# Kernel tuning notes

Measured on AMD Instinct MI355X. Metric: run time of the kernel, lower is better.

Reference implementation:

```python
import jax, jax.numpy as jnp
import numpy as np

EPS = 1e-4

@jax.custom_vjp
def binarize(x):
    # BinaryConnectDeterministic: sign with sign(0)=+1
    return jnp.where(x >= 0, 1.0, -1.0).astype(x.dtype)

def _bin_fwd(x):
    return binarize(x), x

def _bin_bwd(x, g):
    # straight-through estimator, clipped to |x| <= 1
    return (g * (jnp.abs(x) <= 1).astype(g.dtype),)

binarize.defvjp(_bin_fwd, _bin_bwd)

def ap2(x):
    # approximate power-of-2: sign(x) * 2^round(log2|x|); grad is 0 a.e. (round/sign)
    a = jnp.maximum(jnp.abs(x), 1e-38)
    return jnp.sign(x) * jnp.exp2(jnp.round(jnp.log2(a)))

def shift_bn(x, gamma, beta, axes):
    # shift-based batch norm (BNN paper): var approximated via centered*AP2(centered),
    # inverse std and gamma replaced by their AP2 approximations. Training-mode batch stats.
    mean = jnp.mean(x, axis=axes, keepdims=True)
    c = x - mean
    var = jnp.mean(c * ap2(c), axis=axes, keepdims=True)
    xhat = c * ap2(1.0 / jnp.sqrt(var + EPS))
    shape = [1] * x.ndim
    shape[1] = x.shape[1]
    return ap2(gamma.reshape(shape)) * xhat + beta.reshape(shape)

def conv_bin(x, w, b):
    y = jax.lax.conv_general_dilated(x, binarize(w), (1, 1), [(1, 1), (1, 1)],
                                     dimension_numbers=('NCHW', 'OIHW', 'NCHW'))
    return y + b[None, :, None, None]

def maxpool3s2(x):
    return jax.lax.reduce_window(x, -jnp.inf, jax.lax.max,
                                 (1, 1, 3, 3), (1, 1, 2, 2), 'VALID')


def setup_inputs() -> dict:
    key = jax.random.key(0)
    ks = jax.random.split(key, 8)
    B, NU = 2048, 2048
    inp = {
        'x': jax.random.normal(ks[0], (B, 784), jnp.float32),
        'conv1_w': jax.random.normal(ks[1], (32, 1, 3, 3), jnp.float32) * 0.1,
        'conv1_b': jnp.zeros((32,), jnp.float32),
        'g1': jnp.ones((32,), jnp.float32), 'b1': jnp.zeros((32,), jnp.float32),
        'conv2_w': jax.random.normal(ks[2], (64, 32, 3, 3), jnp.float32) * 0.1,
        'conv2_b': jnp.zeros((64,), jnp.float32),
        'g2': jnp.ones((64,), jnp.float32), 'b2': jnp.zeros((64,), jnp.float32),
        'lin3_w': jax.random.normal(ks[3], (NU, 10816), jnp.float32) * 0.02,
        'lin3_b': jnp.zeros((NU,), jnp.float32),
        'g3': jnp.ones((NU,), jnp.float32), 'b3': jnp.zeros((NU,), jnp.float32),
        'lin4_w': jax.random.normal(ks[4], (10, NU), jnp.float32) * 0.02,
        'lin4_b': jnp.zeros((10,), jnp.float32),
    }
    return inp


def reference(x, conv1_w, conv1_b, g1, b1, conv2_w, conv2_b, g2, b2,
              lin3_w, lin3_b, g3, b3, lin4_w, lin4_b):
    h = x.reshape(-1, 1, 28, 28)
    h = jax.nn.relu(conv_bin(h, conv1_w, conv1_b))
    h = shift_bn(h, g1, b1, axes=(0, 2, 3))
    h = binarize(h)
    h = jax.nn.relu(conv_bin(h, conv2_w, conv2_b))
    h = maxpool3s2(h)                       # [B,64,13,13]
    h = shift_bn(h, g2, b2, axes=(0, 2, 3))
    h = binarize(h)
    h = h.reshape(h.shape[0], -1)           # [B,10816]
    h = jax.nn.relu(h @ binarize(lin3_w).T + lin3_b)
    h = shift_bn(h, g3, b3, axes=(0,))
    h = binarize(h)
    return h @ binarize(lin4_w).T + lin4_b  # [B,10] (no norm4/logsoftmax in forward)
```

## Files before the change

### kernel.cpp

```cpp
#include <hip/hip_runtime.h>

#define BB 2048
#define IMG 784
#define HWD 28
#define C1 32
#define C2 64
#define PP 169
#define PD 13
#define F3 10816
#define N3 2048
#define K4W 32
#define NOUT 10
#define CONV 27
#define PADW 30
#define OCCHUNK 8
#define IMGC 29
#define SCRP 740

typedef unsigned long long u64;
typedef int v4i __attribute__((ext_vector_type(4)));
typedef int v16i __attribute__((ext_vector_type(16)));

#define GLOAD16(gp, lp) __builtin_amdgcn_global_load_lds( \
    (__attribute__((address_space(1))) void*)(gp),        \
    (__attribute__((address_space(3))) void*)(lp), 16, 0, 0)

__device__ __forceinline__ float ap2mag(float c) {
    unsigned int a = __float_as_uint(c) & 0x7fffffffu;
    unsigned int e = (a >> 23) + ((a & 0x7fffffu) > 0x3504f3u);
    return __uint_as_float(e << 23);
}
__device__ __forceinline__ float ap2sgn(float g) {
    unsigned int u = __float_as_uint(g);
    unsigned int a = u & 0x7fffffffu;
    if (a == 0) return 0.f;
    unsigned int e = (a >> 23) + ((a & 0x7fffffu) > 0x3504f3u);
    return __uint_as_float((u & 0x80000000u) | (e << 23));
}

__global__ __launch_bounds__(256) void stage0(const float* __restrict__ x,
                                              const float* __restrict__ w1, const float* __restrict__ cb1,
                                              float* __restrict__ part1, float* __restrict__ w1b,
                                              const float* __restrict__ w2, char* __restrict__ w2i8,
                                              const float* __restrict__ w3, char* __restrict__ wp3i,
                                              const float* __restrict__ w4, u64* __restrict__ wp4) {
    __shared__ float xs[30 * PADW];
    __shared__ float red[4 * C1];
    int n = blockIdx.x, tid = threadIdx.x;
    int lane = tid & 63, wv = tid >> 6;
    {
        int idx = n * 256 + tid;
        int nthr = gridDim.x * 256;
        int total = (N3 * F3) / 4;
        for (int t = idx; t < total; t += nthr) {
            float4 wv4 = *(const float4*)(w3 + (size_t)t * 4);
            unsigned int w = (wv4.x >= 0.f ? 0x01u : 0xffu)
                           | (wv4.y >= 0.f ? 0x01u : 0xffu) << 8
                           | (wv4.z >= 0.f ? 0x01u : 0xffu) << 16
                           | (wv4.w >= 0.f ? 0x01u : 0xffu) << 24;
            *(unsigned int*)(wp3i + (size_t)t * 4) = w;
        }
    }
    if (n == 0) {
        for (int i = tid; i < C1 * 9; i += 256) w1b[i] = (w1[i] >= 0.f) ? 1.f : -1.f;
    } else if (n == 1) {
        for (int i = tid; i < 2 * 9 * 64 * 16; i += 256) {
            int hf = i / 9216;
            int r = i - hf * 9216;
            int t = r >> 10;
            int l = (r >> 4) & 63;
            int j = i & 15;
            int oc = hf * 32 + (l & 31);
            int ic = ((l >> 5) << 4) + j;
            w2i8[i] = (w2[oc * 288 + ic * 9 + t] >= 0.f) ? (char)1 : (char)(-1);
        }
    } else if (n == 2) {
        for (int w = wv; w < NOUT * K4W; w += 4) {
            int o = w / K4W, j = w % K4W;
            float wvl = w4[o * N3 + j * 64 + lane];
            u64 mask = __ballot(wvl >= 0.f);
            if (lane == 0) wp4[w] = mask;
        }
    }
    for (int i = tid; i < 30 * PADW; i += 256) {
        int r = i / PADW - 1, c = i % PADW - 1;
        float v = 0.f;
        if (r >= 0 && r < HWD && c >= 0 && c < HWD) v = x[n * IMG + r * HWD + c];
        xs[i] = v;
    }
    __syncthreads();
    bool act = tid < 196;
    int r = tid / 7, c0 = (tid % 7) * 4;
    float win[18];
#pragma unroll
    for (int k = 0; k < 18; k++) win[k] = 0.f;
    if (act) {
#pragma unroll
        for (int ry = 0; ry < 3; ry++)
#pragma unroll
            for (int cx = 0; cx < 6; cx++)
                win[ry * 6 + cx] = xs[(r + ry) * PADW + c0 + cx];
    }
#pragma unroll
    for (int ch = 0; ch < C1; ch++) {
        float a = 0.f;
        if (act) {
            float k0 = (w1[ch * 9 + 0] >= 0.f) ? 1.f : -1.f, k1 = (w1[ch * 9 + 1] >= 0.f) ? 1.f : -1.f;
            float k2 = (w1[ch * 9 + 2] >= 0.f) ? 1.f : -1.f, k3 = (w1[ch * 9 + 3] >= 0.f) ? 1.f : -1.f;
            float k4 = (w1[ch * 9 + 4] >= 0.f) ? 1.f : -1.f, k5 = (w1[ch * 9 + 5] >= 0.f) ? 1.f : -1.f;
            float k6 = (w1[ch * 9 + 6] >= 0.f) ? 1.f : -1.f, k7 = (w1[ch * 9 + 7] >= 0.f) ? 1.f : -1.f;
            float k8 = (w1[ch * 9 + 8] >= 0.f) ? 1.f : -1.f;
            float b = cb1[ch];
#pragma unroll
            for (int px = 0; px < 4; px++) {
                float s = win[px] * k0 + win[px + 1] * k1 + win[px + 2] * k2
                        + win[6 + px] * k3 + win[7 + px] * k4 + win[8 + px] * k5
                        + win[12 + px] * k6 + win[13 + px] * k7 + win[14 + px] * k8;
                a += fmaxf(s + b, 0.f);
            }
        }
        for (int off = 32; off; off >>= 1) a += __shfl_down(a, off);
        if (lane == 0) red[wv * C1 + ch] = a;
    }
    __syncthreads();
    if (tid < C1) part1[n * C1 + tid] = red[tid] + red[C1 + tid] + red[2 * C1 + tid] + red[3 * C1 + tid];
}

__global__ __launch_bounds__(256) void conv1_var(const float* __restrict__ x,
                            const float* __restrict__ w1b,
                            const float* __restrict__ cb1, const float* __restrict__ mean1,
                            float* __restrict__ part) {
    __shared__ float xs[30 * PADW];
    __shared__ float red[4 * C1];
    int n = blockIdx.x, tid = threadIdx.x;
    for (int i = tid; i < 30 * PADW; i += 256) {
        int r = i / PADW - 1, c = i % PADW - 1;
        float v = 0.f;
        if (r >= 0 && r < HWD && c >= 0 && c < HWD) v = x[n * IMG + r * HWD + c];
        xs[i] = v;
    }
    __syncthreads();
    bool act = tid < 196;
    int r = tid / 7, c0 = (tid % 7) * 4;
    float win[18];
#pragma unroll
    for (int k = 0; k < 18; k++) win[k] = 0.f;
    if (act) {
#pragma unroll
        for (int ry = 0; ry < 3; ry++)
#pragma unroll
            for (int cx = 0; cx < 6; cx++)
                win[ry * 6 + cx] = xs[(r + ry) * PADW + c0 + cx];
    }
    int lane = tid & 63, wv = tid >> 6;
#pragma unroll
    for (int ch = 0; ch < C1; ch++) {
        float a = 0.f;
        if (act) {
            float k0 = w1b[ch * 9 + 0], k1 = w1b[ch * 9 + 1], k2 = w1b[ch * 9 + 2];
            float k3 = w1b[ch * 9 + 3], k4 = w1b[ch * 9 + 4], k5 = w1b[ch * 9 + 5];
            float k6 = w1b[ch * 9 + 6], k7 = w1b[ch * 9 + 7], k8 = w1b[ch * 9 + 8];
            float b = cb1[ch], m = mean1[ch];
#pragma unroll
            for (int px = 0; px < 4; px++) {
                float s = win[px] * k0 + win[px + 1] * k1 + win[px + 2] * k2
                        + win[6 + px] * k3 + win[7 + px] * k4 + win[8 + px] * k5
                        + win[12 + px] * k6 + win[13 + px] * k7 + win[14 + px] * k8;
                float v = fmaxf(s + b, 0.f);
                float c = v - m;
                a += fabsf(c) * ap2mag(c);
            }
        }
        for (int off = 32; off; off >>= 1) a += __shfl_down(a, off);
        if (lane == 0) red[wv * C1 + ch] = a;
    }
    __syncthreads();
    if (tid < C1) part[n * C1 + tid] = red[tid] + red[C1 + tid] + red[2 * C1 + tid] + red[3 * C1 + tid];
}

__global__ __launch_bounds__(256) void conv1_pack(const float* __restrict__ x,
                           const float* __restrict__ w1b,
                           const float* __restrict__ cb1, const float* __restrict__ mean1,
                           const float* __restrict__ scale1, const float* __restrict__ beta1,
                           unsigned int* __restrict__ s1p) {
    __shared__ float xs[30 * PADW];
    int n = blockIdx.x, tid = threadIdx.x;
    for (int i = tid; i < 30 * PADW; i += 256) {
        int r = i / PADW - 1, c = i % PADW - 1;
        float v = 0.f;
        if (r >= 0 && r < HWD && c >= 0 && c < HWD) v = x[n * IMG + r * HWD + c];
        xs[i] = v;
    }
    __syncthreads();
    if (tid >= 196) return;
    int r = tid / 7, c0 = (tid % 7) * 4;
    float win[18];
#pragma unroll
    for (int ry = 0; ry < 3; ry++)
#pragma unroll
        for (int cx = 0; cx < 6; cx++)
            win[ry * 6 + cx] = xs[(r + ry) * PADW + c0 + cx];
    unsigned int bits0 = 0, bits1 = 0, bits2 = 0, bits3 = 0;
#pragma unroll
    for (int ch = 0; ch < C1; ch++) {
        float k0 = w1b[ch * 9 + 0], k1 = w1b[ch * 9 + 1], k2 = w1b[ch * 9 + 2];
        float k3 = w1b[ch * 9 + 3], k4 = w1b[ch * 9 + 4], k5 = w1b[ch * 9 + 5];
        float k6 = w1b[ch * 9 + 6], k7 = w1b[ch * 9 + 7], k8 = w1b[ch * 9 + 8];
        float b = cb1[ch], m = mean1[ch], sc = scale1[ch], bt = beta1[ch];
#pragma unroll
        for (int px = 0; px < 4; px++) {
            float s = win[px] * k0 + win[px + 1] * k1 + win[px + 2] * k2
                    + win[6 + px] * k3 + win[7 + px] * k4 + win[8 + px] * k5
                    + win[12 + px] * k6 + win[13 + px] * k7 + win[14 + px] * k8;
            float v = fmaxf(s + b, 0.f);
            float val = sc * (v - m) + bt;
            unsigned int bit = (val >= 0.f ? 1u : 0u) << ch;
            if (px == 0) bits0 |= bit;
            else if (px == 1) bits1 |= bit;
            else if (px == 2) bits2 |= bit;
            else bits3 |= bit;
        }
    }
    uint4 w4v = make_uint4(bits0, bits1, bits2, bits3);
    *reinterpret_cast<uint4*>(&s1p[n * IMG + r * HWD + c0]) = w4v;
}

__global__ __launch_bounds__(256) void conv2pool(const unsigned int* __restrict__ s1p,
                                                 const char* __restrict__ w2i8,
                                                 const float* __restrict__ cb2,
                                                 short* __restrict__ p2i,
                                                 float* __restrict__ part2) {
    __shared__ char img[IMGC * IMGC * 32];
    __shared__ short scr[32 * SCRP];
    __shared__ float psum[OCCHUNK * PP];
    __shared__ float pm[C2];
    int n = blockIdx.x, tid = threadIdx.x;
    int lane = tid & 63, wv = tid >> 6;
    for (int i = tid; i < IMGC * IMGC; i += 256) {
        int r = i / IMGC, c = i - r * IMGC;
        unsigned int w = 0u;
        if (r >= 1 && c >= 1) w = s1p[n * IMG + (r - 1) * HWD + (c - 1)];
        unsigned int d[8];
        if (r == 0 || c == 0) {
#pragma unroll
            for (int e = 0; e < 8; e++) d[e] = 0u;
        } else {
#pragma unroll
            for (int e = 0; e < 8; e++) {
                unsigned int nib = (w >> (4 * e)) & 0xFu;
                unsigned int t = (nib & 1u) | ((nib & 2u) << 7) | ((nib & 4u) << 14) | ((nib & 8u) << 21);
                d[e] = 0xFFFFFFFFu - t * 0xFEu;
            }
        }
        *(uint4*)&img[i * 32] = make_uint4(d[0], d[1], d[2], d[3]);
        *(uint4*)&img[i * 32 + 16] = make_uint4(d[4], d[5], d[6], d[7]);
    }
    __syncthreads();
    int hh = lane >> 5;
    int l31 = lane & 31;
    for (int hf = 0; hf < 2; hf++) {
        v4i bf[9];
#pragma unroll
        for (int t = 0; t < 9; t++)
            bf[t] = *(const v4i*)(w2i8 + (hf * 9 + t) * 1024 + lane * 16);
#pragma unroll
        for (int j = 0; j < 3; j++) {
            int mtA = wv + 8 * j, mtB = mtA + 4;
            int pA = mtA * 32 + l31; if (pA > 728) pA = 728;
            int pB = mtB * 32 + l31; if (pB > 728) pB = 728;
            int yA = pA / 27, xA = pA - yA * 27;
            int yB = pB / 27, xB = pB - yB * 27;
            int aA = (yA * IMGC + xA) * 32 + hh * 16;
            int aB = (yB * IMGC + xB) * 32 + hh * 16;
            v16i accA = {0,0,0,0,0,0,0,0,0,0,0,0,0,0,0,0};
            v16i accB = {0,0,0,0,0,0,0,0,0,0,0,0,0,0,0,0};
#pragma unroll
            for (int ky = 0; ky < 3; ky++)
#pragma unroll
                for (int kx = 0; kx < 3; kx++) {
                    v4i fA = *(const v4i*)&img[aA + (ky * IMGC + kx) * 32];
                    v4i fB = *(const v4i*)&img[aB + (ky * IMGC + kx) * 32];
                    accA = __builtin_amdgcn_mfma_i32_32x32x32_i8(fA, bf[ky * 3 + kx], accA, 0, 0, 0);
                    accB = __builtin_amdgcn_mfma_i32_32x32x32_i8(fB, bf[ky * 3 + kx], accB, 0, 0, 0);
                }
            short* sr = &scr[l31 * SCRP];
#pragma unroll
            for (int g = 0; g < 4; g++) {
                short4 sA;
                sA.x = (short)accA[4 * g + 0]; sA.y = (short)accA[4 * g + 1];
                sA.z = (short)accA[4 * g + 2]; sA.w = (short)accA[4 * g + 3];
                *(short4*)&sr[mtA * 32 + g * 8 + 4 * hh] = sA;
            }
            if (mtB < 23) {
#pragma unroll
                for (int g = 0; g < 4; g++) {
                    short4 sB;
                    sB.x = (short)accB[4 * g + 0]; sB.y = (short)accB[4 * g + 1];
                    sB.z = (short)accB[4 * g + 2]; sB.w = (short)accB[4 * g + 3];
                    *(short4*)&sr[mtB * 32 + g * 8 + 4 * hh] = sB;
                }
            }
        }
        __syncthreads();
        for (int base = 0; base < 32; base += OCCHUNK) {
            for (int q = tid; q < OCCHUNK * PP; q += 256) {
                int ol = q / PP, pix = q - ol * PP;
                int py = pix / PD, px = pix - py * PD;
                const short* rr = &scr[(base + ol) * SCRP + (2 * py) * CONV + 2 * px];
                int m0 = max(max((int)rr[0], (int)rr[1]), (int)rr[2]);
                int m1 = max(max((int)rr[CONV], (int)rr[CONV + 1]), (int)rr[CONV + 2]);
                int m2 = max(max((int)rr[2 * CONV], (int)rr[2 * CONV + 1]), (int)rr[2 * CONV + 2]);
                int val = max(max(m0, m1), m2);
                int oc = hf * 32 + base + ol;
                p2i[n * F3 + oc * PP + pix] = (short)val;
                psum[q] = fmaxf((float)val + cb2[oc], 0.f);
            }
            __syncthreads();
            for (int ol = wv; ol < OCCHUNK; ol += 4) {
                float a = 0.f;
                for (int pp = lane; pp < PP; pp += 64) a += psum[ol * PP + pp];
                for (int off = 32; off; off >>= 1) a += __shfl_down(a, off);
                if (lane == 0) pm[hf * 32 + base + ol] = a;
            }
            __syncthreads();
        }
    }
    if (tid < C2) part2[n * C2 + tid] = pm[tid];
}

__global__ __launch_bounds__(256) void p2_var(const short* __restrict__ p2i,
                         const float* __restrict__ cb2,
                         const float* __restrict__ mean2, float* __restrict__ part) {
    int n = blockIdx.x, tid = threadIdx.x, lane = tid & 63, wv = tid >> 6;
    const short* rowb = p2i + (size_t)n * F3;
    __shared__ float red[C2];
#pragma unroll
    for (int i = 0; i < 16; i++) {
        int ch = wv * 16 + i;
        const short* row = rowb + ch * PP;
        float b = cb2[ch];
        float m = mean2[ch];
        float a = 0.f;
        for (int p = lane; p < PP; p += 64) {
            float v = fmaxf((float)row[p] + b, 0.f);
            float c = v - m;
            a += fabsf(c) * ap2mag(c);
        }
        for (int off = 32; off; off >>= 1) a += __shfl_down(a, off);
        if (lane == 0) red[ch] = a;
    }
    __syncthreads();
    if (tid < C2) part[n * C2 + tid] = red[tid];
}

__global__ __launch_bounds__(256) void reduce_stats(const float* __restrict__ part, int nch, int nblk,
                             const float* __restrict__ g, float* __restrict__ outv,
                             int mode, double count) {
    int ch = blockIdx.x, tid = threadIdx.x;
    double a = 0.0;
    for (int i = tid; i < nblk; i += 256) a += (double)part[(size_t)i * nch + ch];
    __shared__ double red[4];
    for (int off = 32; off; off >>= 1) a += __shfl_down(a, off);
    int lane = tid & 63, wv = tid >> 6;
    if (lane == 0) red[wv] = a;
    __syncthreads();
    if (tid == 0) {
        double s = red[0] + red[1] + red[2] + red[3];
        if (mode == 0) {
            outv[ch] = (float)(s / count);
        } else {
            float var = (float)(s / count);
            float inv = 1.0f / sqrtf(var + 1e-4f);
            outv[ch] = ap2sgn(g[ch]) * ap2mag(inv);
        }
    }
}

__global__ __launch_bounds__(256) void p2_packi8(const short* __restrict__ p2i, const float* __restrict__ cb2,
                        const float* __restrict__ mean2, const float* __restrict__ scale2,
                        const float* __restrict__ beta2, char* __restrict__ hp3i) {
    int idx = blockIdx.x * 256 + threadIdx.x;
    int nthr = gridDim.x * 256;
    int total = (BB * F3) / 4;
    for (int t = idx; t < total; t += nthr) {
        int base = t * 4;
        int f0 = base % F3;
        unsigned int w = 0;
#pragma unroll
        for (int e = 0; e < 4; e++) {
            int f = f0 + e;
            int oc = f / PP;
            float v = fmaxf((float)p2i[base + e] + cb2[oc], 0.f);
            float val = scale2[oc] * (v - mean2[oc]) + beta2[oc];
            w |= (val >= 0.f ? 0x01u : 0xffu) << (8 * e);
        }
        *(unsigned int*)(hp3i + base) = w;
    }
}

__global__ __launch_bounds__(256) void lin3_mfma(const char* __restrict__ hp3i,
                                                 const char* __restrict__ wp3i,
                                                 const float* __restrict__ b3l,
                                                 float* __restrict__ h3,
                                                 float* __restrict__ h3T,
                                                 float* __restrict__ part3) {
    __shared__ v4i aL[2][1024];
    __shared__ v4i bL[2][512];
    __shared__ float csr[4][32];
    int tid = threadIdx.x;
    int lane = tid & 63, wv = tid >> 6;
    int wr = wv >> 1, wc = wv & 1;
    int m0 = blockIdx.y * 128, n0 = blockIdx.x * 64;
    int loff = (lane & 15) * F3 + (lane >> 4) * 16;
    const char* gA0 = hp3i + (size_t)(m0 + wv * 16) * F3 + loff;
    const char* gA1 = gA0 + (size_t)64 * F3;
    const char* gB0 = wp3i + (size_t)(n0 + wv * 16) * F3 + loff;
    char* ldsA = (char*)&aL[0][0];
    char* ldsB = (char*)&bL[0][0];
    int sA = wv * 1024, sB = wv * 1024;
    v4i acc[4][2];
#pragma unroll
    for (int i = 0; i < 4; i++)
#pragma unroll
        for (int j = 0; j < 2; j++) acc[i][j] = (v4i){0, 0, 0, 0};
    GLOAD16(gA0,      ldsA + sA);
    GLOAD16(gA1,      ldsA + sA + 4096);
    GLOAD16(gA0 + 64, ldsA + sA + 8192);
    GLOAD16(gA1 + 64, ldsA + sA + 12288);
    GLOAD16(gB0,      ldsB + sB);
    GLOAD16(gB0 + 64, ldsB + sB + 4096);
    __syncthreads();
    for (int c = 0; c <= 84; ++c) {
        int cur = c & 1;
        if (c < 84) {
            int nb = cur ^ 1;
            const char* pA0 = gA0 + (size_t)(c + 1) * 128;
            const char* pA1 = gA1 + (size_t)(c + 1) * 128;
            const char* pB0 = gB0 + (size_t)(c + 1) * 128;
            char* dA = ldsA + nb * 16384 + sA;
            char* dB = ldsB + nb * 8192 + sB;
            GLOAD16(pA0, dA);
            GLOAD16(pA1, dA + 4096);
            GLOAD16(pB0, dB);
            if (c + 1 < 84) {
                GLOAD16(pA0 + 64, dA + 8192);
                GLOAD16(pA1 + 64, dA + 12288);
                GLOAD16(pB0 + 64, dB + 4096);
            }
        }
        const v4i* aC = &aL[cur][0];
        const v4i* bC = &bL[cur][0];
        int nks = (c == 84) ? 1 : 2;
        for (int ks = 0; ks < nks; ++ks) {
            v4i af[4], bf[2];
#pragma unroll
            for (int i = 0; i < 4; i++) af[i] = aC[ks * 512 + (wr * 4 + i) * 64 + lane];
#pragma unroll
            for (int j = 0; j < 2; j++) bf[j] = bC[ks * 256 + (wc * 2 + j) * 64 + lane];
#pragma unroll
            for (int i = 0; i < 4; i++)
#pragma unroll
                for (int j = 0; j < 2; j++)
                    acc[i][j] = __builtin_amdgcn_mfma_i32_16x16x64_i8(af[i], bf[j], acc[i][j], 0, 0, 0);
        }
        __syncthreads();
    }
    int q = lane >> 4, m16 = lane & 15;
    float cs[2] = {0.f, 0.f};
#pragma unroll
    for (int j = 0; j < 2; j++) {
        int col = n0 + wc * 32 + j * 16 + m16;
        float bias = b3l[col];
#pragma unroll
        for (int i = 0; i < 4; i++) {
            int rowb = m0 + wr * 64 + i * 16 + q * 4;
            float4 t4;
#pragma unroll
            for (int rg = 0; rg < 4; rg++) {
                float v = fmaxf((float)acc[i][j][rg] + bias, 0.f);
                h3[(size_t)(rowb + rg) * N3 + col] = v;
                ((float*)&t4)[rg] = v;
                cs[j] += v;
            }
            *(float4*)&h3T[(size_t)col * BB + rowb] = t4;
        }
    }
#pragma unroll
    for (int j = 0; j < 2; j++) {
        cs[j] += __shfl_xor(cs[j], 16);
        cs[j] += __shfl_xor(cs[j], 32);
        if (lane < 16) csr[wv][j * 16 + m16] = cs[j];
    }
    __syncthreads();
    if (tid < 64) {
        int wcc = tid >> 5, cc = tid & 31;
        part3[(size_t)blockIdx.y * N3 + n0 + tid] = csr[wcc][cc] + csr[2 + wcc][cc];
    }
}

__global__ __launch_bounds__(256) void h3_finish(const float* __restrict__ h3T,
                                                 const float* __restrict__ part3,
                                                 const float* __restrict__ g3,
                                                 float* __restrict__ mean3, float* __restrict__ scale3) {
    int nn = blockIdx.x, tid = threadIdx.x;
    __shared__ float msh;
    __shared__ double redd[4];
    if (tid < 64) {
        float a = (tid < 16) ? part3[(size_t)tid * N3 + nn] : 0.f;
        for (int off = 8; off; off >>= 1) a += __shfl_down(a, off);
        if (tid == 0) { float m = a / (float)BB; mean3[nn] = m; msh = m; }
    }
    __syncthreads();
    float m = msh;
    float acc = 0.f;
#pragma unroll
    for (int q = 0; q < 8; q++) {
        float v = h3T[(size_t)nn * BB + q * 256 + tid];
        float c = v - m;
        acc += fabsf(c) * ap2mag(c);
    }
    double a = (double)acc;
    for (int off = 32; off; off >>= 1) a += __shfl_down(a, off);
    int lane = tid & 63, wv = tid >> 6;
    if (lane == 0) redd[wv] = a;
    __syncthreads();
    if (tid == 0) {
        float var = (float)((redd[0] + redd[1] + redd[2] + redd[3]) / (double)BB);
        float inv = 1.0f / sqrtf(var + 1e-4f);
        scale3[nn] = ap2sgn(g3[nn]) * ap2mag(inv);
    }
}

__global__ __launch_bounds__(256) void h4_out(const float* __restrict__ h3,
                                              const float* __restrict__ mean3, const float* __restrict__ scale3,
                                              const float* __restrict__ bt3,
                                              const u64* __restrict__ wp4, const float* __restrict__ b4,
                                              float* __restrict__ out) {
    __shared__ u64 hb[K4W];
    __shared__ u64 wsh[NOUT * 33];
    int m = blockIdx.x, tid = threadIdx.x, lane = tid & 63, wv = tid >> 6;
    for (int i = tid; i < NOUT * K4W; i += 256) wsh[(i / K4W) * 33 + (i % K4W)] = wp4[i];
#pragma unroll
    for (int q = 0; q < 8; q++) {
        int j = wv * 8 + q;
        int f = j * 64 + lane;
        float v = h3[(size_t)m * N3 + f];
        float val = scale3[f] * (v - mean3[f]) + bt3[f];
        u64 mask = __ballot(val >= 0.f);
        if (lane == 0) hb[j] = mask;
    }
    __syncthreads();
    if (tid < NOUT) {
        int c = 0;
#pragma unroll
        for (int k = 0; k < K4W; k++) c += (int)__popcll(hb[k] ^ wsh[tid * 33 + k]);
        out[m * NOUT + tid] = (float)(N3 - 2 * c) + b4[tid];
    }
}

extern "C" void kernel_launch(void* const* d_in, const int* in_sizes, int n_in,
                              void* d_out, int out_size, void* d_ws, size_t ws_size,
                              hipStream_t stream) {
    const float* x   = (const float*)d_in[0];
    const float* w1  = (const float*)d_in[1];
    const float* cb1 = (const float*)d_in[2];
    const float* g1  = (const float*)d_in[3];
    const float* bt1 = (const float*)d_in[4];
    const float* w2  = (const float*)d_in[5];
    const float* cb2 = (const float*)d_in[6];
    const float* g2  = (const float*)d_in[7];
    const float* bt2 = (const float*)d_in[8];
    const float* w3  = (const float*)d_in[9];
    const float* b3l = (const float*)d_in[10];
    const float* g3  = (const float*)d_in[11];
    const float* bt3 = (const float*)d_in[12];
    const float* w4  = (const float*)d_in[13];
    const float* b4l = (const float*)d_in[14];
    float* out = (float*)d_out;

    char* base = (char*)d_ws;
    size_t off = 0;
    auto carve = [&](size_t bytes) { char* p = base + off; off = (off + bytes + 255) & ~(size_t)255; return p; };
    char* bufA = carve((size_t)BB * C2 * PP * 2);
    char* bufB = carve((size_t)BB * F3);
    char* bufC = carve((size_t)N3 * F3);
    short* p2i         = (short*)bufA;
    float* h3          = (float*)bufA;
    float* h3T         = (float*)(bufA + (size_t)BB * N3 * 4);
    char* hp3i         = bufB;
    unsigned int* s1p  = (unsigned int*)bufB;
    char* wp3i         = bufC;
    u64* wp4           = (u64*)carve((size_t)NOUT * K4W * 8);
    char* w2i8         = (char*)carve((size_t)2 * 9 * 64 * 16);
    float* w1b         = (float*)carve((size_t)C1 * 9 * 4);
    float* part1       = (float*)carve((size_t)BB * C1 * 4);
    float* part2       = (float*)carve((size_t)BB * C2 * 4);
    float* part3       = (float*)carve((size_t)16 * N3 * 4);
    float* fstats      = (float*)carve((size_t)(32 + 32 + 64 + 64 + 2048 + 2048) * 4);
    float* mean1 = fstats;          float* scale1 = fstats + 32;
    float* mean2 = fstats + 64;     float* scale2 = fstats + 128;
    float* mean3 = fstats + 192;    float* scale3 = fstats + 2240;

    stage0<<<BB, 256, 0, stream>>>(x, w1, cb1, part1, w1b, w2, w2i8, w3, wp3i, w4, wp4);
    reduce_stats<<<C1, 256, 0, stream>>>(part1, C1, BB, g1, mean1, 0, (double)BB * IMG);
    conv1_var<<<BB, 256, 0, stream>>>(x, w1b, cb1, mean1, part1);
    reduce_stats<<<C1, 256, 0, stream>>>(part1, C1, BB, g1, scale1, 1, (double)BB * IMG);
    conv1_pack<<<BB, 256, 0, stream>>>(x, w1b, cb1, mean1, scale1, bt1, s1p);
    conv2pool<<<BB, 256, 0, stream>>>(s1p, w2i8, cb2, p2i, part2);
    reduce_stats<<<C2, 256, 0, stream>>>(part2, C2, BB, g2, mean2, 0, (double)BB * PP);
    p2_var<<<BB, 256, 0, stream>>>(p2i, cb2, mean2, part2);
    reduce_stats<<<C2, 256, 0, stream>>>(part2, C2, BB, g2, scale2, 1, (double)BB * PP);
    p2_packi8<<<2048, 256, 0, stream>>>(p2i, cb2, mean2, scale2, bt2, hp3i);
    lin3_mfma<<<dim3(32, 16), 256, 0, stream>>>(hp3i, wp3i, b3l, h3, h3T, part3);
    h3_finish<<<N3, 256, 0, stream>>>(h3T, part3, g3, mean3, scale3);
    h4_out<<<BB, 256, 0, stream>>>(h3, mean3, scale3, bt3, wp4, b4l, out);

    (void)in_sizes; (void)n_in; (void)out_size; (void)ws_size;
}
```

Measured before the change: 549.9 us.

## Triple-buffer lin3 int8 MFMA K-loop with explicit vmcnt waits and setprio

Replaces the double-buffered LDS pipeline in the lin3 int8 GEMM with a three-stage ring buffer. Loads are issued two chunks ahead, and the loop waits with an explicit `s_waitcnt vmcnt(6)` plus a raw `s_barrier` instead of `__syncthreads`, so global-to-LDS copies overlap more of the MFMA work. MFMA bursts are wrapped in `s_setprio` to favour the math waves. In exchange it uses more LDS per block, which may lower occupancy. The final staged chunk now loads a full 128 bytes, which reads 64 bytes past the end of each row and past the end of the buffer for the last rows.

Measured after the change: 549.3 us. Within noise of the previous version (-0.1%).

```diff
diff --git a/kernel.cpp b/kernel.cpp
--- a/kernel.cpp
+++ b/kernel.cpp
@@ -404,8 +404,8 @@
                                                  float* __restrict__ h3,
                                                  float* __restrict__ h3T,
                                                  float* __restrict__ part3) {
-    __shared__ v4i aL[2][1024];
-    __shared__ v4i bL[2][512];
+    __shared__ v4i aL[3][1024];
+    __shared__ v4i bL[3][512];
     __shared__ float csr[4][32];
     int tid = threadIdx.x;
     int lane = tid & 63, wv = tid >> 6;
@@ -417,54 +417,65 @@
     const char* gB0 = wp3i + (size_t)(n0 + wv * 16) * F3 + loff;
     char* ldsA = (char*)&aL[0][0];
     char* ldsB = (char*)&bL[0][0];
-    int sA = wv * 1024, sB = wv * 1024;
+    int sA = wv * 1024;
     v4i acc[4][2];
 #pragma unroll
     for (int i = 0; i < 4; i++)
 #pragma unroll
         for (int j = 0; j < 2; j++) acc[i][j] = (v4i){0, 0, 0, 0};
-    GLOAD16(gA0,      ldsA + sA);
-    GLOAD16(gA1,      ldsA + sA + 4096);
-    GLOAD16(gA0 + 64, ldsA + sA + 8192);
-    GLOAD16(gA1 + 64, ldsA + sA + 12288);
-    GLOAD16(gB0,      ldsB + sB);
-    GLOAD16(gB0 + 64, ldsB + sB + 4096);
-    __syncthreads();
-    for (int c = 0; c <= 84; ++c) {
-        int cur = c & 1;
-        if (c < 84) {
-            int nb = cur ^ 1;
-            const char* pA0 = gA0 + (size_t)(c + 1) * 128;
-            const char* pA1 = gA1 + (size_t)(c + 1) * 128;
-            const char* pB0 = gB0 + (size_t)(c + 1) * 128;
-            char* dA = ldsA + nb * 16384 + sA;
-            char* dB = ldsB + nb * 8192 + sB;
-            GLOAD16(pA0, dA);
-            GLOAD16(pA1, dA + 4096);
-            GLOAD16(pB0, dB);
-            if (c + 1 < 84) {
-                GLOAD16(pA0 + 64, dA + 8192);
-                GLOAD16(pA1 + 64, dA + 12288);
-                GLOAD16(pB0 + 64, dB + 4096);
-            }
-        }
+
+    auto stage = [&](int c) {
+        int b = c % 3;
+        const char* pA0 = gA0 + (size_t)c * 128;
+        const char* pA1 = gA1 + (size_t)c * 128;
+        const char* pB0 = gB0 + (size_t)c * 128;
+        char* dA = ldsA + b * 16384 + sA;
+        char* dB = ldsB + b * 8192 + sA;
+        GLOAD16(pA0, dA);
+        GLOAD16(pA1, dA + 4096);
+        GLOAD16(pA0 + 64, dA + 8192);
+        GLOAD16(pA1 + 64, dA + 12288);
+        GLOAD16(pB0, dB);
+        GLOAD16(pB0 + 64, dB + 4096);
+    };
+    auto compute = [&](int c, int nks) {
+        int cur = c % 3;
         const v4i* aC = &aL[cur][0];
         const v4i* bC = &bL[cur][0];
-        int nks = (c == 84) ? 1 : 2;
         for (int ks = 0; ks < nks; ++ks) {
             v4i af[4], bf[2];
 #pragma unroll
             for (int i = 0; i < 4; i++) af[i] = aC[ks * 512 + (wr * 4 + i) * 64 + lane];
 #pragma unroll
             for (int j = 0; j < 2; j++) bf[j] = bC[ks * 256 + (wc * 2 + j) * 64 + lane];
+            __builtin_amdgcn_s_setprio(1);
 #pragma unroll
             for (int i = 0; i < 4; i++)
 #pragma unroll
                 for (int j = 0; j < 2; j++)
                     acc[i][j] = __builtin_amdgcn_mfma_i32_16x16x64_i8(af[i], bf[j], acc[i][j], 0, 0, 0);
-        }
-        __syncthreads();
-    }
+            __builtin_amdgcn_s_setprio(0);
+        }
+    };
+
+    stage(0);
+    stage(1);
+    asm volatile("s_waitcnt vmcnt(6)" ::: "memory");
+    __builtin_amdgcn_s_barrier();
+    __builtin_amdgcn_sched_barrier(0);
+    for (int c = 0; c < 83; ++c) {
+        stage(c + 2);
+        compute(c, 2);
+        asm volatile("s_waitcnt vmcnt(6)" ::: "memory");
+        __builtin_amdgcn_s_barrier();
+        __builtin_amdgcn_sched_barrier(0);
+    }
+    compute(83, 2);
+    asm volatile("s_waitcnt vmcnt(0)" ::: "memory");
+    __builtin_amdgcn_s_barrier();
+    __builtin_amdgcn_sched_barrier(0);
+    compute(84, 1);
+
     int q = lane >> 4, m16 = lane & 15;
     float cs[2] = {0.f, 0.f};
 #pragma unroll
```
